# Performance work log

Hardware: AMD Instinct MI355X
Metric: run time of the kernel (lower is better)

The kernel has to match this reference:

```python
import jax, jax.numpy as jnp
import numpy as np

B, T, D = 16, 512, 256          # batch, seq_len, d_model (= num features = num graph nodes N)
H, MC, K, DE, DH = 4, 4, 3, 10, 128
GS, SS, AS = 4, 6, 4            # global/sector/asset regime states
TAU = 0.5
STEPS = 3                       # diffusion steps
HID = max(64, D)
DEC_H = max(64, D // 2)


def setup_inputs() -> dict:
    key = jax.random.key(0)
    ks = iter(jax.random.split(key, 64))

    def nrm(shape, s=0.02):
        return (s * jax.random.normal(next(ks), shape)).astype(jnp.float32)

    z = lambda *s: jnp.zeros(s, jnp.float32)
    o = lambda *s: jnp.ones(s, jnp.float32)
    p = dict(
        x=jax.random.normal(next(ks), (B, T, D), dtype=jnp.float32),
        # hierarchical regime controller
        gW1=nrm((D, HID)), gb1=z(HID), g_ln_w=o(HID), g_ln_b=z(HID),
        gW2=nrm((HID, GS)), gb2=z(GS),
        sW1=nrm((D, HID)), sb1=z(HID), sW2=nrm((HID, D * SS)), sb2=z(D * SS),
        aW1=nrm((D, HID)), ab1=z(HID), aW2=nrm((HID, D * AS)), ab2=z(D * AS),
        global_prior=z(GS), sector_prior=z(SS), asset_prior=z(AS),
        g2f=nrm((GS, D)),
        sector_emb=jax.random.normal(next(ks), (SS, D), dtype=jnp.float32),
        asset_emb=jax.random.normal(next(ks), (AS, D), dtype=jnp.float32),
        # bidirectional temporal scan (BI-Mamba stand-in)
        decay_f=nrm((D,), 1.0), decay_b=nrm((D,), 1.0),
        tW=nrm((D, D)), tb=z(D),
        # Bayesian MAGAC + diffusion graph prior
        psi=nrm((H, D, DE), 0.1), log_sigma=jnp.full((H,), -2.0, jnp.float32),
        step_logits=jnp.linspace(-1.0, 0.5, STEPS).astype(jnp.float32),
        noise_scale=jnp.full((STEPS,), 0.05, jnp.float32),
        Wk=nrm((K + 1, T, DH)),
        mean_w=nrm((DH,)), mean_b=z(), lv_w=nrm((DH,)), lv_b=z(),
        # risk-aware decoder
        dW1=nrm((D, DEC_H)), db1=z(DEC_H), d_ln_w=o(DEC_H), d_ln_b=z(DEC_H),
        mW=nrm((DEC_H,)), mb=z(), lvW=nrm((DEC_H,)), lvb=z(),
        cW=nrm((DEC_H,)), cb=z(),
    )
    return p


def _ln(h, w, b):
    m = h.mean(-1, keepdims=True)
    v = h.var(-1, keepdims=True)  # biased, matches torch LayerNorm
    return (h - m) / jnp.sqrt(v + 1e-5) * w + b


def _gelu(h):
    return jax.nn.gelu(h, approximate=False)


def _gumbel_softmax(k, logits):
    u = jax.random.uniform(k, logits.shape, minval=1e-6, maxval=1.0 - 1e-6)
    g = -jnp.log(-jnp.log(u))
    return jax.nn.softmax((logits + g) / TAU, axis=-1)


def _fwd(x, gW1, gb1, g_ln_w, g_ln_b, gW2, gb2, sW1, sb1, sW2, sb2,
         aW1, ab1, aW2, ab2, global_prior, sector_prior, asset_prior,
         g2f, sector_emb, asset_emb, decay_f, decay_b, tW, tb,
         psi, log_sigma, step_logits, noise_scale, Wk,
         mean_w, mean_b, lv_w, lv_b,
         dW1, db1, d_ln_w, d_ln_b, mW, mb, lvW, lvb, cW, cb):
    rk = jax.random.key(42)
    k_g, k_s, k_a, k_eps, k_diff = jax.random.split(rk, 5)

    # ---- hierarchical regime controller ----
    seq_mean = x.mean(1)                               # (B, D)
    diff_summary = (x[:, 1:] - x[:, :-1]).mean(1)      # (B, D)
    g_logits = _gelu(_ln(seq_mean @ gW1 + gb1, g_ln_w, g_ln_b)) @ gW2 + gb2
    s_logits = (_gelu(seq_mean @ sW1 + sb1) @ sW2 + sb2).reshape(B, D, SS)
    a_logits = (_gelu(diff_summary @ aW1 + ab1) @ aW2 + ab2).reshape(B, D, AS)
    g_probs = _gumbel_softmax(k_g, g_logits)
    s_probs = _gumbel_softmax(k_s, s_logits)
    a_probs = _gumbel_softmax(k_a, a_logits)
    global_gate = g_probs @ g2f                                   # (B, D)
    # diagonal of einsum('bfs,sd->bfd') == einsum('bfs,sf->bf')
    sector_gate = jnp.einsum('bfs,sf->bf', s_probs, sector_emb)
    asset_gate = jnp.einsum('bfs,sf->bf', a_probs, asset_emb)
    feature_gate = jax.nn.sigmoid(global_gate + sector_gate + asset_gate)
    gated_x = x * feature_gate[:, None, :]

    # ---- bidirectional temporal EMA scan (BI-Mamba stand-in) ----
    af = jax.nn.sigmoid(decay_f)
    abk = jax.nn.sigmoid(decay_b)
    xs = gated_x.transpose(1, 0, 2)                    # (T, B, D)

    def ema(a):
        def step(h, xt):
            h = a * h + (1.0 - a) * xt
            return h, h
        return step

    _, hf = jax.lax.scan(ema(af), jnp.zeros_like(xs[0]), xs)
    _, hb = jax.lax.scan(ema(abk), jnp.zeros_like(xs[0]), xs[::-1])
    temporal = (hf + hb[::-1]).transpose(1, 0, 2) @ tW + tb       # (B, T, D)
    node_major = temporal.transpose(0, 2, 1)                      # (B, N=D, T)

    # ---- Bayesian adjacency sampling (MC samples per head) ----
    logits = jnp.einsum('hne,hme->hnm', psi, psi) / jnp.sqrt(jnp.float32(DE))
    sigma = jnp.exp(log_sigma)                                    # (H,)
    eps = jax.random.normal(k_eps, (MC, H, D, D))
    A = jax.nn.softmax(logits[None] + sigma[None, :, None, None] * eps, axis=-1)

    # ---- diffusion refinement guided by regime features ----
    ctx = feature_gate.mean(0)
    ctx = ctx / (jnp.linalg.norm(ctx) + 1e-6)
    outer = ctx[:, None] * ctx[None, :]
    outer = outer / jnp.maximum(outer.sum(-1, keepdims=True), 1e-6)
    dkeys = jax.random.split(k_diff, STEPS)
    for s in range(STEPS):                             # fixed small loop, vectorized over (MC,H)
        alpha = jax.nn.sigmoid(step_logits[s])
        noise = noise_scale[s] * jax.random.normal(dkeys[s], A.shape)
        A = alpha * A + (1.0 - alpha) * outer + noise
        A = 0.5 * (A + jnp.swapaxes(A, -1, -2))
        A = jax.nn.softmax(A, axis=-1)

    # ---- K-hop graph conv, averaged over MC samples and heads ----
    Z = jnp.einsum('bnt,td->bnd', node_major, Wk[0])[None, None]  # hop 0
    P = jnp.broadcast_to(node_major, (MC, H, B, D, T))
    for k in range(1, K + 1):
        P = jnp.einsum('mhnp,mhbpt->mhbnt', A, P)
        Z = Z + jnp.einsum('mhbnt,td->mhbnd', P, Wk[k])
    Z = Z.mean((0, 1))                                            # (B, N, DH)
    graph_mean = Z @ mean_w + mean_b                              # (B, N)
    graph_logvar = Z @ lv_w + lv_b                                # (B, N)

    # ---- risk-aware decoder ----
    feat = _ln(_gelu(graph_mean @ dW1 + db1), d_ln_w, d_ln_b)     # (B, DEC_H)
    mean = feat @ mW + mb
    dec_logvar = feat @ lvW + lvb
    _cvar = jax.nn.sigmoid(feat @ cW + cb)  # auxiliary head (not in returned output)
    var = jnp.exp(dec_logvar) + jnp.exp(graph_logvar).sum(1)
    log_var = jnp.log(var)
    return jnp.stack([mean, log_var], axis=-1)                    # (B, 2)


def reference(x, gW1, gb1, g_ln_w, g_ln_b, gW2, gb2, sW1, sb1, sW2, sb2,
              aW1, ab1, aW2, ab2, global_prior, sector_prior, asset_prior,
              g2f, sector_emb, asset_emb, decay_f, decay_b, tW, tb,
              psi, log_sigma, step_logits, noise_scale, Wk,
              mean_w, mean_b, lv_w, lv_b,
              dW1, db1, d_ln_w, d_ln_b, mW, mb, lvW, lvb, cW, cb):
    return _fwd(x, gW1, gb1, g_ln_w, g_ln_b, gW2, gb2, sW1, sb1, sW2, sb2,
                aW1, ab1, aW2, ab2, global_prior, sector_prior, asset_prior,
                g2f, sector_emb, asset_emb, decay_f, decay_b, tW, tb,
                psi, log_sigma, step_logits, noise_scale, Wk,
                mean_w, mean_b, lv_w, lv_b,
                dW1, db1, d_ln_w, d_ln_b, mW, mb, lvW, lvb, cW, cb)
```

## Files before the change

### kernel.cpp

```cpp
#include <hip/hip_runtime.h>
#include <stdint.h>

#define PARTITIONABLE 1

namespace {

struct TFPair { uint32_t a, b; };

__host__ __device__ constexpr uint32_t rotl32(uint32_t x, int d) {
  return (x << d) | (x >> (32 - d));
}

__host__ __device__ constexpr TFPair tf2x32(uint32_t k0, uint32_t k1,
                                            uint32_t x0, uint32_t x1) {
  uint32_t k2 = k0 ^ k1 ^ 0x1BD11BDAu;
  x0 += k0; x1 += k1;
  x0 += x1; x1 = rotl32(x1, 13); x1 ^= x0;
  x0 += x1; x1 = rotl32(x1, 15); x1 ^= x0;
  x0 += x1; x1 = rotl32(x1, 26); x1 ^= x0;
  x0 += x1; x1 = rotl32(x1, 6);  x1 ^= x0;
  x0 += k1; x1 += k2 + 1u;
  x0 += x1; x1 = rotl32(x1, 17); x1 ^= x0;
  x0 += x1; x1 = rotl32(x1, 29); x1 ^= x0;
  x0 += x1; x1 = rotl32(x1, 16); x1 ^= x0;
  x0 += x1; x1 = rotl32(x1, 24); x1 ^= x0;
  x0 += k2; x1 += k0 + 2u;
  x0 += x1; x1 = rotl32(x1, 13); x1 ^= x0;
  x0 += x1; x1 = rotl32(x1, 15); x1 ^= x0;
  x0 += x1; x1 = rotl32(x1, 26); x1 ^= x0;
  x0 += x1; x1 = rotl32(x1, 6);  x1 ^= x0;
  x0 += k0; x1 += k1 + 3u;
  x0 += x1; x1 = rotl32(x1, 17); x1 ^= x0;
  x0 += x1; x1 = rotl32(x1, 29); x1 ^= x0;
  x0 += x1; x1 = rotl32(x1, 16); x1 ^= x0;
  x0 += x1; x1 = rotl32(x1, 24); x1 ^= x0;
  x0 += k1; x1 += k2 + 4u;
  x0 += x1; x1 = rotl32(x1, 13); x1 ^= x0;
  x0 += x1; x1 = rotl32(x1, 15); x1 ^= x0;
  x0 += x1; x1 = rotl32(x1, 26); x1 ^= x0;
  x0 += x1; x1 = rotl32(x1, 6);  x1 ^= x0;
  x0 += k2; x1 += k0 + 5u;
  return TFPair{x0, x1};
}

#if PARTITIONABLE
constexpr TFPair KG  = tf2x32(0u, 42u, 0u, 0u);
constexpr TFPair KS  = tf2x32(0u, 42u, 0u, 1u);
constexpr TFPair KA  = tf2x32(0u, 42u, 0u, 2u);
constexpr TFPair KE  = tf2x32(0u, 42u, 0u, 3u);
constexpr TFPair KD  = tf2x32(0u, 42u, 0u, 4u);
constexpr TFPair DK0 = tf2x32(KD.a, KD.b, 0u, 0u);
constexpr TFPair DK1 = tf2x32(KD.a, KD.b, 0u, 1u);
constexpr TFPair DK2 = tf2x32(KD.a, KD.b, 0u, 2u);
#else
constexpr TFPair SP0 = tf2x32(0u, 42u, 0u, 5u);
constexpr TFPair SP1 = tf2x32(0u, 42u, 1u, 6u);
constexpr TFPair SP2 = tf2x32(0u, 42u, 2u, 7u);
constexpr TFPair SP3 = tf2x32(0u, 42u, 3u, 8u);
constexpr TFPair SP4 = tf2x32(0u, 42u, 4u, 9u);
constexpr TFPair KG  = TFPair{SP0.a, SP1.a};
constexpr TFPair KS  = TFPair{SP2.a, SP3.a};
constexpr TFPair KA  = TFPair{SP4.a, SP0.b};
constexpr TFPair KE  = TFPair{SP1.b, SP2.b};
constexpr TFPair KD  = TFPair{SP3.b, SP4.b};
constexpr TFPair DP0 = tf2x32(KD.a, KD.b, 0u, 3u);
constexpr TFPair DP1 = tf2x32(KD.a, KD.b, 1u, 4u);
constexpr TFPair DP2 = tf2x32(KD.a, KD.b, 2u, 5u);
constexpr TFPair DK0 = TFPair{DP0.a, DP1.a};
constexpr TFPair DK1 = TFPair{DP2.a, DP0.b};
constexpr TFPair DK2 = TFPair{DP1.b, DP2.b};
#endif

__device__ __forceinline__ uint32_t rbits(uint32_t k0, uint32_t k1,
                                          uint32_t idx, uint32_t half) {
#if PARTITIONABLE
  TFPair t = tf2x32(k0, k1, 0u, idx);
  return t.a ^ t.b;
#else
  if (idx < half) return tf2x32(k0, k1, idx, idx + half).a;
  return tf2x32(k0, k1, idx - half, idx).b;
#endif
}

__device__ __forceinline__ float bits_to_u01(uint32_t bits) {
  return __uint_as_float((bits >> 9) | 0x3F800000u) - 1.0f;
}

__device__ __forceinline__ float gumbel_u(uint32_t k0, uint32_t k1,
                                          uint32_t idx, uint32_t half) {
  const float mn = 1e-6f;
  const float mx = 1.0f - 1e-6f;
  float f = bits_to_u01(rbits(k0, k1, idx, half));
  return fmaxf(mn, f * (mx - mn) + mn);
}

__device__ __forceinline__ float erfinv_f32(float x) {
  float w = -log1pf(-x * x);
  float p;
  if (w < 5.0f) {
    w -= 2.5f;
    p = 2.81022636e-08f;
    p = fmaf(p, w, 3.43273939e-07f);
    p = fmaf(p, w, -3.5233877e-06f);
    p = fmaf(p, w, -4.39150654e-06f);
    p = fmaf(p, w, 0.00021858087f);
    p = fmaf(p, w, -0.00125372503f);
    p = fmaf(p, w, -0.00417768164f);
    p = fmaf(p, w, 0.246640727f);
    p = fmaf(p, w, 1.50140941f);
  } else {
    w = sqrtf(w) - 3.0f;
    p = -0.000200214257f;
    p = fmaf(p, w, 0.000100950558f);
    p = fmaf(p, w, 0.00134934322f);
    p = fmaf(p, w, -0.00367342844f);
    p = fmaf(p, w, 0.00573950773f);
    p = fmaf(p, w, -0.0076224613f);
    p = fmaf(p, w, 0.00943887047f);
    p = fmaf(p, w, 1.00167406f);
    p = fmaf(p, w, 2.83297682f);
  }
  return p * x;
}

__device__ __forceinline__ float normal_from(uint32_t k0, uint32_t k1,
                                             uint32_t idx, uint32_t half) {
  const float lo = -0x1.fffffep-1f;
  float f = bits_to_u01(rbits(k0, k1, idx, half));
  float u = fmaxf(lo, f * 2.0f + lo);
  return 1.41421356237f * erfinv_f32(u);
}

__device__ __forceinline__ float gelu_f(float x) {
  return 0.5f * x * (1.0f + erff(x / 1.4142135623730951f));
}
__device__ __forceinline__ float sigmoid_f(float x) {
  return 1.0f / (1.0f + expf(-x));
}

__device__ __forceinline__ float wave_sum(float v) {
  #pragma unroll
  for (int m = 32; m > 0; m >>= 1) v += __shfl_xor(v, m);
  return v;
}
__device__ __forceinline__ float wave_max(float v) {
  #pragma unroll
  for (int m = 32; m > 0; m >>= 1) v = fmaxf(v, __shfl_xor(v, m));
  return v;
}
template <int NW>
__device__ __forceinline__ float blk_sum(float v, float* slots) {
  v = wave_sum(v);
  int wid = threadIdx.x >> 6;
  if ((threadIdx.x & 63) == 0) slots[wid] = v;
  __syncthreads();
  float r = slots[0];
  #pragma unroll
  for (int i = 1; i < NW; ++i) r += slots[i];
  return r;
}
template <int NW>
__device__ __forceinline__ float blk_max(float v, float* slots) {
  v = wave_max(v);
  int wid = threadIdx.x >> 6;
  if ((threadIdx.x & 63) == 0) slots[wid] = v;
  __syncthreads();
  float r = slots[0];
  #pragma unroll
  for (int i = 1; i < NW; ++i) r = fmaxf(r, slots[i]);
  return r;
}

struct Params {
  const float *x, *gW1, *gb1, *glnw, *glnb, *gW2, *gb2, *sW1, *sb1, *sW2, *sb2,
      *aW1, *ab1, *aW2, *ab2, *g2f, *semb, *aemb, *decay_f, *decay_b, *tW, *tb,
      *psi, *log_sigma, *step_logits, *noise_scale, *Wk, *mean_w, *mean_b,
      *lv_w, *lv_b, *dW1, *db1, *dlnw, *dlnb, *mW, *mb, *lvW, *lvb;
  float* out;
  float *fg, *ctx, *v, *sv, *u, *Pf, *Qf, *Pb, *Qb, *Lf, *Lb, *YH,
      *R1, *gm, *glv, *A, *A2, *At, *At2, *hgS, *hgA, *lvS, *lvA, *gpv;
};


__device__ __forceinline__ void phase_w1head(const Params& P, float* smem,
                                             int blk, int tid) {
  float* src  = smem;
  float* s1   = smem + 256;
  float* s2   = smem + 260;
  float* gsl  = smem + 264;
  float* gvals= smem + 280;
  int head = blk >> 4, b = blk & 15;
  const float* xb = P.x + (size_t)b * 512 * 256 + tid;
  if (head < 2) {
    float s = 0.f;
    for (int tc = 0; tc < 16; ++tc) {
      float ps = 0.f;
      #pragma unroll
      for (int i = 0; i < 32; ++i) ps += xb[(size_t)(tc * 32 + i) * 256];
      s += ps;
    }
    src[tid] = s / 512.0f;
  } else {
    src[tid] = (xb[(size_t)511 * 256] - xb[0]) / 511.0f;
  }
  __syncthreads();
  const float* W = (head == 0) ? P.gW1 : (head == 1) ? P.sW1 : P.aW1;
  const float* bias = (head == 0) ? P.gb1 : (head == 1) ? P.sb1 : P.ab1;
  float acc = bias[tid];
  #pragma unroll 8
  for (int d = 0; d < 256; ++d)
    acc = fmaf(src[d], W[(size_t)d * 256 + tid], acc);
  if (head == 1) { P.hgS[b * 256 + tid] = gelu_f(acc); return; }
  if (head == 2) { P.hgA[b * 256 + tid] = gelu_f(acc); return; }
  float mean = blk_sum<4>(acc, s1) / 256.0f;
  float dv = acc - mean;
  float var = blk_sum<4>(dv * dv, s2) / 256.0f;
  float hg = gelu_f(dv / sqrtf(var + 1e-5f) * P.glnw[tid] + P.glnb[tid]);
  float lg[4];
  #pragma unroll
  for (int sx = 0; sx < 4; ++sx)
    lg[sx] = blk_sum<4>(hg * P.gW2[tid * 4 + sx], gsl + 4 * sx);
  if (tid < 4) {
    float u = gumbel_u(KG.a, KG.b, (uint32_t)(b * 4 + tid), 32u);
    float g = -logf(-logf(u));
    gvals[tid] = (lg[tid] + P.gb2[tid] + g) / 0.5f;
  }
  __syncthreads();
  if (tid < 4) {
    float mx = fmaxf(fmaxf(gvals[0], gvals[1]), fmaxf(gvals[2], gvals[3]));
    float sum = expf(gvals[0] - mx) + expf(gvals[1] - mx) +
                expf(gvals[2] - mx) + expf(gvals[3] - mx);
    P.gpv[b * 4 + tid] = expf(gvals[tid] - mx) / sum;
  }
}

__device__ __forceinline__ void phase_l2gemm(const Params& P, float* smem,
                                             int blk, int tid) {
  float* h = smem;
  if (blk < 96) {
    int b = blk / 6, ct = blk % 6;
    h[tid] = P.hgS[b * 256 + tid];
    __syncthreads();
    int col = ct * 256 + tid;
    float acc = P.sb2[col];
    const float* wp = P.sW2 + col;
    #pragma unroll 8
    for (int d = 0; d < 256; ++d) acc = fmaf(h[d], wp[(size_t)d * 1536], acc);
    int f = col / 6, sx = col - f * 6;
    float u = gumbel_u(KS.a, KS.b, (uint32_t)(b * 256 + f) * 6u + sx, 12288u);
    P.lvS[b * 1536 + col] = (acc + (-logf(-logf(u)))) / 0.5f;
  } else {
    int idx = blk - 96;
    int b = idx >> 2, ct = idx & 3;
    h[tid] = P.hgA[b * 256 + tid];
    __syncthreads();
    int col = ct * 256 + tid;
    float acc = P.ab2[col];
    const float* wp = P.aW2 + col;
    #pragma unroll 8
    for (int d = 0; d < 256; ++d) acc = fmaf(h[d], wp[(size_t)d * 1024], acc);
    int f = col >> 2, sx = col & 3;
    float u = gumbel_u(KA.a, KA.b, (uint32_t)(b * 256 + f) * 4u + sx, 8192u);
    P.lvA[b * 1024 + col] = (acc + (-logf(-logf(u)))) / 0.5f;
  }
}

__device__ __forceinline__ void phase_gfin(const Params& P, int b, int tid) {
  int f = tid;
  const float* lvSb = P.lvS + b * 1536 + f * 6;
  float v0 = lvSb[0], v1 = lvSb[1], v2 = lvSb[2];
  float v3 = lvSb[3], v4 = lvSb[4], v5 = lvSb[5];
  float mx = fmaxf(fmaxf(fmaxf(v0, v1), fmaxf(v2, v3)), fmaxf(v4, v5));
  float e0 = expf(v0 - mx), e1 = expf(v1 - mx), e2 = expf(v2 - mx);
  float e3 = expf(v3 - mx), e4 = expf(v4 - mx), e5 = expf(v5 - mx);
  float ssum = e0 + e1 + e2 + e3 + e4 + e5;
  float sg = (e0 / ssum) * P.semb[0 * 256 + f] + (e1 / ssum) * P.semb[1 * 256 + f] +
             (e2 / ssum) * P.semb[2 * 256 + f] + (e3 / ssum) * P.semb[3 * 256 + f] +
             (e4 / ssum) * P.semb[4 * 256 + f] + (e5 / ssum) * P.semb[5 * 256 + f];
  const float* lvAb = P.lvA + b * 1024 + f * 4;
  float a0 = lvAb[0], a1 = lvAb[1], a2 = lvAb[2], a3 = lvAb[3];
  float amx = fmaxf(fmaxf(a0, a1), fmaxf(a2, a3));
  float x0 = expf(a0 - amx), x1 = expf(a1 - amx);
  float x2 = expf(a2 - amx), x3 = expf(a3 - amx);
  float asum = x0 + x1 + x2 + x3;
  float ag = (x0 / asum) * P.aemb[0 * 256 + f] + (x1 / asum) * P.aemb[1 * 256 + f] +
             (x2 / asum) * P.aemb[2 * 256 + f] + (x3 / asum) * P.aemb[3 * 256 + f];
  float gg = 0.f;
  #pragma unroll
  for (int sx = 0; sx < 4; ++sx) gg = fmaf(P.gpv[b * 4 + sx], P.g2f[sx * 256 + f], gg);
  P.fg[b * 256 + f] = sigmoid_f(gg + sg + ag);
}

__device__ __forceinline__ void phase_vcompute(const Params& P, int bid2,
                                               int tid) {
  int j = bid2 >> 2, tg = bid2 & 3;
  const float* wp = (j & 1) ? P.lv_w : P.mean_w;
  const float* Wkk = P.Wk + (size_t)(j >> 1) * 65536;
  int wid = tid >> 6, lane = tid & 63;
  float w0 = wp[lane], w1 = wp[64 + lane];
  float svloc = 0.f;
  for (int i = 0; i < 32; ++i) {
    int t = tg * 128 + wid * 32 + i;
    const float* row = Wkk + (size_t)t * 128;
    float s = row[lane] * w0 + row[64 + lane] * w1;
    s = wave_sum(s);
    if (lane == 0) { P.v[j * 512 + t] = s; svloc += s; }
  }
  if (lane == 0) P.sv[j * 16 + tg * 4 + wid] = svloc;
}

__device__ __forceinline__ void phase_ainit_row(const Params& P, float* smem,
                                                int blk, int tid) {
  float* pn = smem;
  float* s1 = smem + 12;
  float* s2 = smem + 16;
  int mh = blk >> 8, h = mh & 3, n = blk & 255, p = tid;
  if (p < 10) pn[p] = P.psi[(size_t)(h * 256 + n) * 10 + p];
  __syncthreads();
  const float* pp = P.psi + (size_t)(h * 256 + p) * 10;
  float s = 0.f;
  #pragma unroll
  for (int e = 0; e < 10; ++e) s = fmaf(pn[e], pp[e], s);
  float logit = s / sqrtf(10.0f);
  uint32_t idx = (uint32_t)blk * 256u + (uint32_t)p;
  float eps = normal_from(KE.a, KE.b, idx, 524288u);
  float val = logit + expf(P.log_sigma[h]) * eps;
  float mx = blk_max<4>(val, s1);
  float e = expf(val - mx);
  float sum = blk_sum<4>(e, s2);
  P.A[(size_t)blk * 256 + p] = e / sum;
}

__device__ __forceinline__ void phase_ctx(const Params& P, float* smem,
                                          int tid) {
  float* s1 = smem;
  float* s2 = smem + 4;
  float c = 0.f;
  for (int b = 0; b < 16; ++b) c += P.fg[b * 256 + tid];
  c /= 16.0f;
  float ss = blk_sum<4>(c * c, s1);
  float cv = c / (sqrtf(ss) + 1e-6f);
  P.ctx[tid] = cv;
  float S = blk_sum<4>(cv, s2);
  if (tid == 0) P.ctx[256] = S;
}

__device__ __forceinline__ void phase_transA(const Params& P, float* smem,
                                             int blk, int tid) {
  float* tile = smem;
  int mh = blk >> 6;
  int tr = ((blk >> 3) & 7) * 32, tc = (blk & 7) * 32;
  const float* src = P.A + (size_t)mh * 65536;
  float* dst = P.At + (size_t)mh * 65536;
  int lr = tid >> 5, lc = tid & 31;
  #pragma unroll
  for (int p = 0; p < 4; ++p) {
    int r = p * 8 + lr;
    tile[r * 33 + lc] = src[(size_t)(tr + r) * 256 + tc + lc];
  }
  __syncthreads();
  #pragma unroll
  for (int p = 0; p < 4; ++p) {
    int r = p * 8 + lr;
    dst[(size_t)(tc + r) * 256 + tr + lc] = tile[lc * 33 + r];
  }
}

__device__ __forceinline__ void phase_scan1(const Params& P, float* smem,
                                            int ch, int tid) {
  float* vv = smem;
  int b = ch >> 4, c = ch & 15;
  int d = tid;
  vv[(d >> 5) * 32 + (d & 31)] = P.v[(d >> 5) * 512 + c * 32 + (d & 31)];
  __syncthreads();
  float g = P.fg[b * 256 + d];
  float af = sigmoid_f(P.decay_f[d]);
  float ab = sigmoid_f(P.decay_b[d]);
  float r_gx[32];
  const float* xp = P.x + ((size_t)b * 512 + c * 32) * 256 + d;
  #pragma unroll
  for (int i = 0; i < 32; ++i) r_gx[i] = xp[(size_t)i * 256] * g;
  float h = 0.f, pw = 1.f;
  float Pr[8], Q[8];
  #pragma unroll
  for (int j = 0; j < 8; ++j) { Pr[j] = 0.f; Q[j] = 0.f; }
  #pragma unroll
  for (int i = 0; i < 32; ++i) {
    h = fmaf(af, h, (1.0f - af) * r_gx[i]);
    pw *= af;
    #pragma unroll
    for (int j = 0; j < 8; ++j) {
      float vj = vv[j * 32 + i];
      Pr[j] = fmaf(h, vj, Pr[j]);
      Q[j] = fmaf(pw, vj, Q[j]);
    }
  }
  size_t base = ((size_t)(b * 16 + c) * 8) * 256 + d;
  #pragma unroll
  for (int j = 0; j < 8; ++j) {
    P.Pf[base + j * 256] = Pr[j];
    P.Qf[base + j * 256] = Q[j];
  }
  P.Lf[(b * 16 + c) * 256 + d] = h;
  h = 0.f; pw = 1.f;
  #pragma unroll
  for (int j = 0; j < 8; ++j) { Pr[j] = 0.f; Q[j] = 0.f; }
  #pragma unroll
  for (int i = 31; i >= 0; --i) {
    h = fmaf(ab, h, (1.0f - ab) * r_gx[i]);
    pw *= ab;
    #pragma unroll
    for (int j = 0; j < 8; ++j) {
      float vj = vv[j * 32 + i];
      Pr[j] = fmaf(h, vj, Pr[j]);
      Q[j] = fmaf(pw, vj, Q[j]);
    }
  }
  #pragma unroll
  for (int j = 0; j < 8; ++j) {
    P.Pb[base + j * 256] = Pr[j];
    P.Qb[base + j * 256] = Q[j];
  }
  P.Lb[(b * 16 + c) * 256 + d] = h;
}

__device__ __forceinline__ void phase_scan2(const Params& P, int blk, int tid) {
  int b = blk >> 3, j = blk & 7;
  int d = tid;
  float af = sigmoid_f(P.decay_f[d]);
  float ab = sigmoid_f(P.decay_b[d]);
  float af32 = af, ab32 = ab;
  #pragma unroll
  for (int q = 0; q < 5; ++q) { af32 *= af32; ab32 *= ab32; }
  float acc = 0.f, H = 0.f;
  for (int c = 0; c < 16; ++c) {
    size_t base = ((size_t)(b * 16 + c) * 8 + j) * 256 + d;
    acc += P.Pf[base] + H * P.Qf[base];
    H = P.Lf[(b * 16 + c) * 256 + d] + af32 * H;
  }
  H = 0.f;
  for (int c = 15; c >= 0; --c) {
    size_t base = ((size_t)(b * 16 + c) * 8 + j) * 256 + d;
    acc += P.Pb[base] + H * P.Qb[base];
    H = P.Lb[(b * 16 + c) * 256 + d] + ab32 * H;
  }
  P.u[(b * 8 + j) * 256 + d] = acc;
}

__device__ __forceinline__ void phase_ygemm(const Params& P, float* smem,
                                            int blk32, int tid) {
  float* As = smem;
  float* Bs = smem + 1056;
  float* svs = smem + 2112;
  int n0 = (blk32 & 7) * 32, m0 = (blk32 >> 3) * 32;
  int tx = tid & 31, ty = tid >> 5;
  if (tid < 8) {
    float ssv = 0.f;
    #pragma unroll
    for (int q = 0; q < 16; ++q) ssv += P.sv[tid * 16 + q];
    svs[tid] = ssv;
  }
  float acc[4] = {0.f, 0.f, 0.f, 0.f};
  for (int k0 = 0; k0 < 256; k0 += 32) {
    #pragma unroll
    for (int l = 0; l < 4; ++l) {
      int e = tid + l * 256, r = e >> 5, cc = e & 31;
      As[r * 33 + cc] = P.u[(size_t)(m0 + r) * 256 + k0 + cc];
      Bs[r * 33 + cc] = P.tW[(size_t)(k0 + r) * 256 + n0 + cc];
    }
    __syncthreads();
    #pragma unroll
    for (int kk = 0; kk < 32; ++kk) {
      float bv = Bs[kk * 33 + tx];
      #pragma unroll
      for (int i = 0; i < 4; ++i)
        acc[i] = fmaf(As[(ty + 8 * i) * 33 + kk], bv, acc[i]);
    }
    __syncthreads();
  }
  int n = n0 + tx;
  float tbn = P.tb[n];
  float mb0 = P.mean_b[0], lb0 = P.lv_b[0];
  #pragma unroll
  for (int i = 0; i < 4; ++i) {
    int row = m0 + ty + 8 * i;
    int b = row >> 3, j = row & 7;
    float val = acc[i] + tbn * svs[j];
    if (j == 0) P.gm[b * 256 + n] = val + mb0;
    else if (j == 1) P.glv[b * 256 + n] = val + lb0;
    else {
      int k = (j >> 1) - 1, proj = j & 1;
      P.YH[k * 8192 + n * 32 + b * 2 + proj] = val;
    }
  }
}

template <bool WRITE_T>
__device__ __forceinline__ void phase_mix4(const Params& P, float* smem,
                                           int sidx, const float* Ain,
                                           const float* AinT, float* Aout,
                                           float* AoutT, uint32_t dk0,
                                           uint32_t dk1, int blk, int tid) {
  float* vals = smem;
  float* slots = smem + 4 * 257;
  int mh = blk >> 6, r0 = (blk & 63) * 4;
  float alpha = sigmoid_f(P.step_logits[sidx]);
  float ns = P.noise_scale[sidx];
  float S = P.ctx[256];
  int c = tid;
  float cp = P.ctx[c];
  const size_t mbase = (size_t)mh * 65536;
  #pragma unroll
  for (int r = 0; r < 4; ++r) {
    int n = r0 + r;
    float cn = P.ctx[n];
    float o_np = (cn * cp) / fmaxf(cn * S, 1e-6f);
    float o_pn = (cp * cn) / fmaxf(cp * S, 1e-6f);
    uint32_t i_np = (uint32_t)(mh * 65536 + n * 256 + c);
    uint32_t i_pn = (uint32_t)(mh * 65536 + c * 256 + n);
    float a_np = Ain[mbase + (size_t)n * 256 + c];
    float a_pn = AinT[mbase + (size_t)n * 256 + c];
    float m_np = alpha * a_np + (1.0f - alpha) * o_np +
                 ns * normal_from(dk0, dk1, i_np, 524288u);
    float m_pn = alpha * a_pn + (1.0f - alpha) * o_pn +
                 ns * normal_from(dk0, dk1, i_pn, 524288u);
    vals[r * 257 + c] = 0.5f * (m_np + m_pn);
  }
  __syncthreads();
  #pragma unroll
  for (int r = 0; r < 4; ++r) {
    float val = vals[r * 257 + c];
    float mx = blk_max<4>(val, slots + r * 8);
    float e = expf(val - mx);
    float sum = blk_sum<4>(e, slots + r * 8 + 4);
    float o = e / sum;
    Aout[mbase + (size_t)(r0 + r) * 256 + c] = o;
    if (WRITE_T) vals[r * 257 + c] = o;
  }
  if (WRITE_T) {
    __syncthreads();
    float t0 = vals[0 * 257 + c], t1 = vals[1 * 257 + c];
    float t2 = vals[2 * 257 + c], t3 = vals[3 * 257 + c];
    float4* dst = (float4*)(AoutT + mbase + (size_t)c * 256 + r0);
    dst[0] = make_float4(t0, t1, t2, t3);
  }
}

__device__ __forceinline__ void phase_findec(const Params& P, float* smem,
                                             int bid, int tid) {
  float* gmv = smem;
  float* sl = smem + 256;
  int b = bid;
  float sm_ = 0.f, sl_ = 0.f;
  for (int mh = 0; mh < 16; ++mh) {
    sm_ += P.R1[(size_t)mh * 8192 + tid * 32 + b * 2];
    sl_ += P.R1[(size_t)mh * 8192 + tid * 32 + b * 2 + 1];
  }
  float gmn = P.gm[b * 256 + tid] + sm_ * (1.0f / 16.0f);
  float gln = P.glv[b * 256 + tid] + sl_ * (1.0f / 16.0f);
  gmv[tid] = gmn;
  float se = expf(gln);
  __syncthreads();
  float sumexp = blk_sum<4>(se, sl);
  float h = 0.f;
  if (tid < 128) {
    h = P.db1[tid];
    for (int n = 0; n < 256; ++n) h = fmaf(gmv[n], P.dW1[n * 128 + tid], h);
    h = gelu_f(h);
  }
  float mean = blk_sum<4>(tid < 128 ? h : 0.f, sl + 4) / 128.0f;
  float dv = (tid < 128) ? h - mean : 0.f;
  float var = blk_sum<4>(dv * dv, sl + 8) / 128.0f;
  float feat = (tid < 128) ? dv / sqrtf(var + 1e-5f) * P.dlnw[tid] + P.dlnb[tid]
                           : 0.f;
  float m_c = blk_sum<4>(tid < 128 ? feat * P.mW[tid] : 0.f, sl + 12) + P.mb[0];
  float lv_c = blk_sum<4>(tid < 128 ? feat * P.lvW[tid] : 0.f, sl + 16) + P.lvb[0];
  if (tid == 0) {
    P.out[b * 2 + 0] = m_c;
    P.out[b * 2 + 1] = logf(expf(lv_c) + sumexp);
  }
}


__global__ __launch_bounds__(256) void kA(Params P) {
  __shared__ float smem[288];
  int bid = blockIdx.x, tid = threadIdx.x;
  if (bid < 48) phase_w1head(P, smem, bid, tid);
  else if (bid < 80) phase_vcompute(P, bid - 48, tid);
  else phase_ainit_row(P, smem, bid - 80, tid);
}

__global__ __launch_bounds__(256) void kL2(Params P) {
  __shared__ float smem[1056];
  int bid = blockIdx.x, tid = threadIdx.x;
  if (bid < 160) phase_l2gemm(P, smem, bid, tid);
  else phase_transA(P, smem, bid - 160, tid);
}

__global__ __launch_bounds__(256) void kGF(Params P) {
  __shared__ float smem[1056];
  int bid = blockIdx.x, tid = threadIdx.x;
  if (bid < 16) phase_gfin(P, bid, tid);
  else phase_transA(P, smem, bid - 16 + 512, tid);
}

__global__ __launch_bounds__(256) void kScan(Params P) {
  __shared__ float smem[256];
  int bid = blockIdx.x, tid = threadIdx.x;
  if (bid < 256) phase_scan1(P, smem, bid, tid);
  else phase_ctx(P, smem, tid);
}

__global__ __launch_bounds__(256) void kM0(Params P) {
  __shared__ float smem[1060];
  int bid = blockIdx.x, tid = threadIdx.x;
  if (bid < 1024)
    phase_mix4<true>(P, smem, 0, P.A, P.At, P.A2, P.At2, DK0.a, DK0.b, bid, tid);
  else
    phase_scan2(P, bid - 1024, tid);
}

__global__ __launch_bounds__(256) void kM1(Params P) {
  __shared__ float smem[2120];
  int bid = blockIdx.x, tid = threadIdx.x;
  if (bid < 1024)
    phase_mix4<true>(P, smem, 1, P.A2, P.At2, P.A, P.At, DK1.a, DK1.b, bid, tid);
  else
    phase_ygemm(P, smem, bid - 1024, tid);
}

__global__ __launch_bounds__(256) void kM2(Params P) {
  __shared__ float smem[1060];
  phase_mix4<false>(P, smem, 2, P.A, P.At, P.A2, nullptr, DK2.a, DK2.b,
                    blockIdx.x, threadIdx.x);
}

__global__ __launch_bounds__(256) void kHor(Params P) {
  __shared__ float Rc[512];
  int bid = blockIdx.x, tid = threadIdx.x;
  int mh = bid >> 4, c0 = (bid & 15) * 2;
  const float* Ab = P.A2 + (size_t)mh * 65536;
  const float4* Arow = (const float4*)(Ab + (size_t)tid * 256);
  const float* Y2 = P.YH + 2 * 8192;
  Rc[tid * 2 + 0] = Y2[tid * 32 + c0 + 0];
  Rc[tid * 2 + 1] = Y2[tid * 32 + c0 + 1];
  __syncthreads();
  #pragma unroll
  for (int hop = 0; hop < 3; ++hop) {
    float acc0 = 0.f, acc1 = 0.f;
    const float4* Rc4 = (const float4*)Rc;
    for (int k4 = 0; k4 < 64; ++k4) {
      float4 a = Arow[k4];
      float4 r01 = Rc4[k4 * 2];
      float4 r23 = Rc4[k4 * 2 + 1];
      acc0 = fmaf(a.x, r01.x, acc0); acc1 = fmaf(a.x, r01.y, acc1);
      acc0 = fmaf(a.y, r01.z, acc0); acc1 = fmaf(a.y, r01.w, acc1);
      acc0 = fmaf(a.z, r23.x, acc0); acc1 = fmaf(a.z, r23.y, acc1);
      acc0 = fmaf(a.w, r23.z, acc0); acc1 = fmaf(a.w, r23.w, acc1);
    }
    if (hop == 0) {
      acc0 += P.YH[8192 + tid * 32 + c0 + 0];
      acc1 += P.YH[8192 + tid * 32 + c0 + 1];
    } else if (hop == 1) {
      acc0 += P.YH[tid * 32 + c0 + 0];
      acc1 += P.YH[tid * 32 + c0 + 1];
    }
    __syncthreads();
    Rc[tid * 2 + 0] = acc0;
    Rc[tid * 2 + 1] = acc1;
    __syncthreads();
  }
  P.R1[(size_t)mh * 8192 + (size_t)tid * 32 + c0 + 0] = Rc[tid * 2 + 0];
  P.R1[(size_t)mh * 8192 + (size_t)tid * 32 + c0 + 1] = Rc[tid * 2 + 1];
}

__global__ __launch_bounds__(256) void kFin(Params P) {
  __shared__ float smem[276];
  phase_findec(P, smem, blockIdx.x, threadIdx.x);
}

constexpr size_t O_FG = 0;
constexpr size_t O_CTX = 4096;
constexpr size_t O_V = 4480;
constexpr size_t O_SV = 8576;
constexpr size_t O_U = 8704;
constexpr size_t O_PF = 41472;
constexpr size_t O_QF = 565760;
constexpr size_t O_PB = 1090048;
constexpr size_t O_QB = 1614336;
constexpr size_t O_LF = 2138624;
constexpr size_t O_LB = 2204160;
constexpr size_t O_YH = 2269696;
constexpr size_t O_R1 = 2294272;
constexpr size_t O_GM = 2425344;
constexpr size_t O_GLV = 2429440;
constexpr size_t O_A = 2433536;
constexpr size_t O_A2 = 3482112;
constexpr size_t O_AT = 4530688;
constexpr size_t O_AT2 = 5579264;
constexpr size_t O_HGS = 6627840;
constexpr size_t O_HGA = 6631936;
constexpr size_t O_LVS = 6636032;
constexpr size_t O_LVA = 6660608;
constexpr size_t O_GPV = 6676992;

}

extern "C" void kernel_launch(void* const* d_in, const int* in_sizes, int n_in,
                              void* d_out, int out_size, void* d_ws,
                              size_t ws_size, hipStream_t stream) {
  (void)in_sizes; (void)n_in; (void)out_size; (void)ws_size;
  float* w = (float*)d_ws;
  Params prm;
  prm.x = (const float*)d_in[0];
  prm.gW1 = (const float*)d_in[1];
  prm.gb1 = (const float*)d_in[2];
  prm.glnw = (const float*)d_in[3];
  prm.glnb = (const float*)d_in[4];
  prm.gW2 = (const float*)d_in[5];
  prm.gb2 = (const float*)d_in[6];
  prm.sW1 = (const float*)d_in[7];
  prm.sb1 = (const float*)d_in[8];
  prm.sW2 = (const float*)d_in[9];
  prm.sb2 = (const float*)d_in[10];
  prm.aW1 = (const float*)d_in[11];
  prm.ab1 = (const float*)d_in[12];
  prm.aW2 = (const float*)d_in[13];
  prm.ab2 = (const float*)d_in[14];
  prm.g2f = (const float*)d_in[18];
  prm.semb = (const float*)d_in[19];
  prm.aemb = (const float*)d_in[20];
  prm.decay_f = (const float*)d_in[21];
  prm.decay_b = (const float*)d_in[22];
  prm.tW = (const float*)d_in[23];
  prm.tb = (const float*)d_in[24];
  prm.psi = (const float*)d_in[25];
  prm.log_sigma = (const float*)d_in[26];
  prm.step_logits = (const float*)d_in[27];
  prm.noise_scale = (const float*)d_in[28];
  prm.Wk = (const float*)d_in[29];
  prm.mean_w = (const float*)d_in[30];
  prm.mean_b = (const float*)d_in[31];
  prm.lv_w = (const float*)d_in[32];
  prm.lv_b = (const float*)d_in[33];
  prm.dW1 = (const float*)d_in[34];
  prm.db1 = (const float*)d_in[35];
  prm.dlnw = (const float*)d_in[36];
  prm.dlnb = (const float*)d_in[37];
  prm.mW = (const float*)d_in[38];
  prm.mb = (const float*)d_in[39];
  prm.lvW = (const float*)d_in[40];
  prm.lvb = (const float*)d_in[41];
  prm.out = (float*)d_out;
  prm.fg = w + O_FG;
  prm.ctx = w + O_CTX;
  prm.v = w + O_V;
  prm.sv = w + O_SV;
  prm.u = w + O_U;
  prm.Pf = w + O_PF;
  prm.Qf = w + O_QF;
  prm.Pb = w + O_PB;
  prm.Qb = w + O_QB;
  prm.Lf = w + O_LF;
  prm.Lb = w + O_LB;
  prm.YH = w + O_YH;
  prm.R1 = w + O_R1;
  prm.gm = w + O_GM;
  prm.glv = w + O_GLV;
  prm.A = w + O_A;
  prm.A2 = w + O_A2;
  prm.At = w + O_AT;
  prm.At2 = w + O_AT2;
  prm.hgS = w + O_HGS;
  prm.hgA = w + O_HGA;
  prm.lvS = w + O_LVS;
  prm.lvA = w + O_LVA;
  prm.gpv = w + O_GPV;

  kA<<<4176, 256, 0, stream>>>(prm);
  kL2<<<672, 256, 0, stream>>>(prm);
  kGF<<<528, 256, 0, stream>>>(prm);
  kScan<<<257, 256, 0, stream>>>(prm);
  kM0<<<1152, 256, 0, stream>>>(prm);
  kM1<<<1056, 256, 0, stream>>>(prm);
  kM2<<<1024, 256, 0, stream>>>(prm);
  kHor<<<256, 256, 0, stream>>>(prm);
  kFin<<<16, 256, 0, stream>>>(prm);
}
```

Baseline: 294.6 us.

## Fuse A transpose into softmax init, inline gate compute, drop kGF launch

The A-initialisation now processes 16 rows per block and writes both A and its transpose At directly via float4 stores, which removes the separate shared-memory transpose phase. The gate fg is recomputed inline wherever it is consumed (ctx and scan), so the kGF kernel and the fg buffer are removed. kL2 shrinks to only the L2 GEMM, cutting one launch and several thousand small blocks. In exchange, the gate math is redone redundantly (16x in ctx, once per scan block), and the At stores are strided by column.

```diff
diff --git a/kernel.cpp b/kernel.cpp
--- a/kernel.cpp
+++ b/kernel.cpp
@@ -177,7 +177,7 @@
       *psi, *log_sigma, *step_logits, *noise_scale, *Wk, *mean_w, *mean_b,
       *lv_w, *lv_b, *dW1, *db1, *dlnw, *dlnb, *mW, *mb, *lvW, *lvb;
   float* out;
-  float *fg, *ctx, *v, *sv, *u, *Pf, *Qf, *Pb, *Qb, *Lf, *Lb, *YH,
+  float *ctx, *v, *sv, *u, *Pf, *Qf, *Pb, *Qb, *Lf, *Lb, *YH,
       *R1, *gm, *glv, *A, *A2, *At, *At2, *hgS, *hgA, *lvS, *lvA, *gpv;
 };
 
@@ -265,8 +265,7 @@
   }
 }
 
-__device__ __forceinline__ void phase_gfin(const Params& P, int b, int tid) {
-  int f = tid;
+__device__ __forceinline__ float fg_compute(const Params& P, int b, int f) {
   const float* lvSb = P.lvS + b * 1536 + f * 6;
   float v0 = lvSb[0], v1 = lvSb[1], v2 = lvSb[2];
   float v3 = lvSb[3], v4 = lvSb[4], v5 = lvSb[5];
@@ -287,8 +286,9 @@
              (x2 / asum) * P.aemb[2 * 256 + f] + (x3 / asum) * P.aemb[3 * 256 + f];
   float gg = 0.f;
   #pragma unroll
-  for (int sx = 0; sx < 4; ++sx) gg = fmaf(P.gpv[b * 4 + sx], P.g2f[sx * 256 + f], gg);
-  P.fg[b * 256 + f] = sigmoid_f(gg + sg + ag);
+  for (int sx = 0; sx < 4; ++sx)
+    gg = fmaf(P.gpv[b * 4 + sx], P.g2f[sx * 256 + f], gg);
+  return sigmoid_f(gg + sg + ag);
 }
 
 __device__ __forceinline__ void phase_vcompute(const Params& P, int bid2,
@@ -309,26 +309,46 @@
   if (lane == 0) P.sv[j * 16 + tg * 4 + wid] = svloc;
 }
 
-__device__ __forceinline__ void phase_ainit_row(const Params& P, float* smem,
-                                                int blk, int tid) {
-  float* pn = smem;
-  float* s1 = smem + 12;
-  float* s2 = smem + 16;
-  int mh = blk >> 8, h = mh & 3, n = blk & 255, p = tid;
-  if (p < 10) pn[p] = P.psi[(size_t)(h * 256 + n) * 10 + p];
-  __syncthreads();
-  const float* pp = P.psi + (size_t)(h * 256 + p) * 10;
-  float s = 0.f;
-  #pragma unroll
-  for (int e = 0; e < 10; ++e) s = fmaf(pn[e], pp[e], s);
-  float logit = s / sqrtf(10.0f);
-  uint32_t idx = (uint32_t)blk * 256u + (uint32_t)p;
-  float eps = normal_from(KE.a, KE.b, idx, 524288u);
-  float val = logit + expf(P.log_sigma[h]) * eps;
-  float mx = blk_max<4>(val, s1);
-  float e = expf(val - mx);
-  float sum = blk_sum<4>(e, s2);
-  P.A[(size_t)blk * 256 + p] = e / sum;
+__device__ __forceinline__ void phase_ainit16(const Params& P, float* smem,
+                                              int blk, int tid) {
+  float* pns = smem;
+  float* slots = smem + 160;
+  int mh = blk >> 4, h = mh & 3, r0 = (blk & 15) * 16;
+  int c = tid;
+  if (tid < 160) {
+    int row = tid / 10, e = tid - row * 10;
+    pns[row * 10 + e] = P.psi[(size_t)(h * 256 + r0 + row) * 10 + e];
+  }
+  float pp[10];
+  {
+    const float* ppg = P.psi + (size_t)(h * 256 + c) * 10;
+    #pragma unroll
+    for (int e = 0; e < 10; ++e) pp[e] = ppg[e];
+  }
+  float lsig = expf(P.log_sigma[h]);
+  __syncthreads();
+  float orow[16];
+  #pragma unroll
+  for (int r = 0; r < 16; ++r) {
+    int n = r0 + r;
+    float s = 0.f;
+    #pragma unroll
+    for (int e = 0; e < 10; ++e) s = fmaf(pns[r * 10 + e], pp[e], s);
+    float logit = s / sqrtf(10.0f);
+    uint32_t idx = (uint32_t)(mh * 256 + n) * 256u + (uint32_t)c;
+    float eps = normal_from(KE.a, KE.b, idx, 524288u);
+    float val = logit + lsig * eps;
+    float mx = blk_max<4>(val, slots + r * 8);
+    float e_ = expf(val - mx);
+    float sum = blk_sum<4>(e_, slots + r * 8 + 4);
+    orow[r] = e_ / sum;
+    P.A[(size_t)mh * 65536 + (size_t)n * 256 + c] = orow[r];
+  }
+  float4* dst = (float4*)(P.At + (size_t)mh * 65536 + (size_t)c * 256 + r0);
+  dst[0] = make_float4(orow[0], orow[1], orow[2], orow[3]);
+  dst[1] = make_float4(orow[4], orow[5], orow[6], orow[7]);
+  dst[2] = make_float4(orow[8], orow[9], orow[10], orow[11]);
+  dst[3] = make_float4(orow[12], orow[13], orow[14], orow[15]);
 }
 
 __device__ __forceinline__ void phase_ctx(const Params& P, float* smem,
@@ -336,7 +356,7 @@
   float* s1 = smem;
   float* s2 = smem + 4;
   float c = 0.f;
-  for (int b = 0; b < 16; ++b) c += P.fg[b * 256 + tid];
+  for (int b = 0; b < 16; ++b) c += fg_compute(P, b, tid);
   c /= 16.0f;
   float ss = blk_sum<4>(c * c, s1);
   float cv = c / (sqrtf(ss) + 1e-6f);
@@ -345,27 +365,6 @@
   if (tid == 0) P.ctx[256] = S;
 }
 
-__device__ __forceinline__ void phase_transA(const Params& P, float* smem,
-                                             int blk, int tid) {
-  float* tile = smem;
-  int mh = blk >> 6;
-  int tr = ((blk >> 3) & 7) * 32, tc = (blk & 7) * 32;
-  const float* src = P.A + (size_t)mh * 65536;
-  float* dst = P.At + (size_t)mh * 65536;
-  int lr = tid >> 5, lc = tid & 31;
-  #pragma unroll
-  for (int p = 0; p < 4; ++p) {
-    int r = p * 8 + lr;
-    tile[r * 33 + lc] = src[(size_t)(tr + r) * 256 + tc + lc];
-  }
-  __syncthreads();
-  #pragma unroll
-  for (int p = 0; p < 4; ++p) {
-    int r = p * 8 + lr;
-    dst[(size_t)(tc + r) * 256 + tr + lc] = tile[lc * 33 + r];
-  }
-}
-
 __device__ __forceinline__ void phase_scan1(const Params& P, float* smem,
                                             int ch, int tid) {
   float* vv = smem;
@@ -373,7 +372,7 @@
   int d = tid;
   vv[(d >> 5) * 32 + (d & 31)] = P.v[(d >> 5) * 512 + c * 32 + (d & 31)];
   __syncthreads();
-  float g = P.fg[b * 256 + d];
+  float g = fg_compute(P, b, d);
   float af = sigmoid_f(P.decay_f[d]);
   float ab = sigmoid_f(P.decay_b[d]);
   float r_gx[32];
@@ -587,21 +586,12 @@
   int bid = blockIdx.x, tid = threadIdx.x;
   if (bid < 48) phase_w1head(P, smem, bid, tid);
   else if (bid < 80) phase_vcompute(P, bid - 48, tid);
-  else phase_ainit_row(P, smem, bid - 80, tid);
+  else phase_ainit16(P, smem, bid - 80, tid);
 }
 
 __global__ __launch_bounds__(256) void kL2(Params P) {
-  __shared__ float smem[1056];
-  int bid = blockIdx.x, tid = threadIdx.x;
-  if (bid < 160) phase_l2gemm(P, smem, bid, tid);
-  else phase_transA(P, smem, bid - 160, tid);
-}
-
-__global__ __launch_bounds__(256) void kGF(Params P) {
-  __shared__ float smem[1056];
-  int bid = blockIdx.x, tid = threadIdx.x;
-  if (bid < 16) phase_gfin(P, bid, tid);
-  else phase_transA(P, smem, bid - 16 + 512, tid);
+  __shared__ float smem[256];
+  phase_l2gemm(P, smem, blockIdx.x, threadIdx.x);
 }
 
 __global__ __launch_bounds__(256) void kScan(Params P) {
@@ -679,30 +669,29 @@
   phase_findec(P, smem, blockIdx.x, threadIdx.x);
 }
 
-constexpr size_t O_FG = 0;
-constexpr size_t O_CTX = 4096;
-constexpr size_t O_V = 4480;
-constexpr size_t O_SV = 8576;
-constexpr size_t O_U = 8704;
-constexpr size_t O_PF = 41472;
-constexpr size_t O_QF = 565760;
-constexpr size_t O_PB = 1090048;
-constexpr size_t O_QB = 1614336;
-constexpr size_t O_LF = 2138624;
-constexpr size_t O_LB = 2204160;
-constexpr size_t O_YH = 2269696;
-constexpr size_t O_R1 = 2294272;
-constexpr size_t O_GM = 2425344;
-constexpr size_t O_GLV = 2429440;
-constexpr size_t O_A = 2433536;
-constexpr size_t O_A2 = 3482112;
-constexpr size_t O_AT = 4530688;
-constexpr size_t O_AT2 = 5579264;
-constexpr size_t O_HGS = 6627840;
-constexpr size_t O_HGA = 6631936;
-constexpr size_t O_LVS = 6636032;
-constexpr size_t O_LVA = 6660608;
-constexpr size_t O_GPV = 6676992;
+constexpr size_t O_CTX = 0;
+constexpr size_t O_V = 384;
+constexpr size_t O_SV = 4480;
+constexpr size_t O_U = 4608;
+constexpr size_t O_PF = 37376;
+constexpr size_t O_QF = 561664;
+constexpr size_t O_PB = 1085952;
+constexpr size_t O_QB = 1610240;
+constexpr size_t O_LF = 2134528;
+constexpr size_t O_LB = 2200064;
+constexpr size_t O_YH = 2265600;
+constexpr size_t O_R1 = 2290176;
+constexpr size_t O_GM = 2421248;
+constexpr size_t O_GLV = 2425344;
+constexpr size_t O_A = 2429440;
+constexpr size_t O_A2 = 3478016;
+constexpr size_t O_AT = 4526592;
+constexpr size_t O_AT2 = 5575168;
+constexpr size_t O_HGS = 6623744;
+constexpr size_t O_HGA = 6627840;
+constexpr size_t O_LVS = 6631936;
+constexpr size_t O_LVA = 6656512;
+constexpr size_t O_GPV = 6672896;
 
 }
 
@@ -752,7 +741,6 @@
   prm.lvW = (const float*)d_in[40];
   prm.lvb = (const float*)d_in[41];
   prm.out = (float*)d_out;
-  prm.fg = w + O_FG;
   prm.ctx = w + O_CTX;
   prm.v = w + O_V;
   prm.sv = w + O_SV;
@@ -777,9 +765,8 @@
   prm.lvA = w + O_LVA;
   prm.gpv = w + O_GPV;
 
-  kA<<<4176, 256, 0, stream>>>(prm);
-  kL2<<<672, 256, 0, stream>>>(prm);
-  kGF<<<528, 256, 0, stream>>>(prm);
+  kA<<<336, 256, 0, stream>>>(prm);
+  kL2<<<160, 256, 0, stream>>>(prm);
   kScan<<<257, 256, 0, stream>>>(prm);
   kM0<<<1152, 256, 0, stream>>>(prm);
   kM1<<<1056, 256, 0, stream>>>(prm);
```

After: 303.1 us. 1.03x slower.
